# Kernel optimization log

Hardware: AMD Instinct MI355X
Metric: run time of the kernel (lower is better)

## Reference

```python
import jax, jax.numpy as jnp
import numpy as np

N_NEIGHBORS = 16


def setup_inputs() -> dict:
    key = jax.random.key(0)
    k1, k2 = jax.random.split(key)
    X_train = jax.random.normal(k1, (65536, 256), dtype=jnp.float32)
    X_test = jax.random.normal(k2, (4096, 256), dtype=jnp.float32)
    return {"X_train": X_train, "X_test": X_test}


def reference(X_train, X_test):
    # Euclidean cdist via ||a||^2 + ||b||^2 - 2 a.b (GEMM-dominant form)
    test_sq = jnp.sum(X_test * X_test, axis=1, keepdims=True)        # [Nt, 1]
    train_sq = jnp.sum(X_train * X_train, axis=1)[None, :]            # [1, Nn]
    cross = X_test @ X_train.T                                        # [Nt, Nn]
    d2 = jnp.maximum(test_sq + train_sq - 2.0 * cross, 0.0)
    dists = jnp.sqrt(d2)                                              # [Nt, Nn]
    # smallest-k == top_k of negated distances (returns ascending distances)
    _, idxs = jax.lax.top_k(-dists, N_NEIGHBORS)                      # [Nt, k]
    return idxs
```

## Files before the change

kernel.cpp:

```cpp
#include <hip/hip_runtime.h>
#include <hip/hip_bf16.h>


typedef short bf16x8 __attribute__((ext_vector_type(8)));
typedef float f32x4 __attribute__((ext_vector_type(4)));
typedef unsigned short ushort_t;
typedef unsigned long long u64;

#define K_DIM     256
#define N_TRAIN   65536
#define N_TEST    4096
#define TM        128
#define TN        128
#define NCHUNK    16
#define CHUNK_N   (N_TRAIN / NCHUNK)
#define ITERS     (CHUNK_N / TN)
#define LISTN     16
#define RPB       8
#define SENT      0xFFFFFFFFu

static __device__ __forceinline__ float np_pw_sq128(const float* __restrict__ x) {
    #pragma clang fp contract(off)
    float r0, r1, r2, r3, r4, r5, r6, r7;
    {
        const float4 a = *(const float4*)(x + 0);
        const float4 b = *(const float4*)(x + 4);
        r0 = a.x * a.x; r1 = a.y * a.y; r2 = a.z * a.z; r3 = a.w * a.w;
        r4 = b.x * b.x; r5 = b.y * b.y; r6 = b.z * b.z; r7 = b.w * b.w;
    }
    for (int i = 8; i < 128; i += 8) {
        const float4 a = *(const float4*)(x + i);
        const float4 b = *(const float4*)(x + i + 4);
        r0 = r0 + a.x * a.x; r1 = r1 + a.y * a.y;
        r2 = r2 + a.z * a.z; r3 = r3 + a.w * a.w;
        r4 = r4 + b.x * b.x; r5 = r5 + b.y * b.y;
        r6 = r6 + b.z * b.z; r7 = r7 + b.w * b.w;
    }
    return ((r0 + r1) + (r2 + r3)) + ((r4 + r5) + (r6 + r7));
}

static __device__ __forceinline__ void gld_lds16(const ushort_t* g, ushort_t* l) {
    __builtin_amdgcn_global_load_lds(
        (const __attribute__((address_space(1))) unsigned int*)g,
        (__attribute__((address_space(3))) unsigned int*)l,
        16, 0, 0);
}

static __device__ __forceinline__ ushort_t f2bf(float x) {
    unsigned u = __float_as_uint(x);
    return (ushort_t)((u + 0x7FFFu + ((u >> 16) & 1u)) >> 16);
}

__global__ __launch_bounds__(256) void convert_bf16(
    const float* __restrict__ src, ushort_t* __restrict__ dst, int nrows)
{
    const int wid = threadIdx.x >> 6, lane = threadIdx.x & 63;
    const int row = blockIdx.x * 4 + wid;
    if (row >= nrows) return;
    const float4 f = *(const float4*)(src + (size_t)row * K_DIM + lane * 4);
    ushort4 h;
    h.x = f2bf(f.x); h.y = f2bf(f.y); h.z = f2bf(f.z); h.w = f2bf(f.w);
    *(ushort4*)(dst + (size_t)row * K_DIM + lane * 4) = h;
}

__global__ __launch_bounds__(256) void train_sq_np(
    const float* __restrict__ train, float* __restrict__ bsq)
{
    const int r = blockIdx.x * 256 + threadIdx.x;
    const float* x = train + (size_t)r * K_DIM;
    bsq[r] = np_pw_sq128(x) + np_pw_sq128(x + 128);
}

__global__ __launch_bounds__(512, 4) void knn_approx(
    const ushort_t* __restrict__ testBf, const ushort_t* __restrict__ trainBf,
    const float* __restrict__ bsq, unsigned* __restrict__ cand)
{
    __shared__ __align__(16) ushort_t sB[TN * 128];
    __shared__ __align__(16) float    sBsq[TN];

    const int tid = threadIdx.x;
    const int bx = blockIdx.x;
    const int chunk = bx & (NCHUNK - 1);
    const int rowTile = bx >> 4;
    const int rowBase = rowTile * TM;
    const int chunkBase = chunk * CHUNK_N;
    const int lane = tid & 63;
    const int wid = tid >> 6;
    const int quad = lane >> 4;
    const int l15 = lane & 15;

    const int myRow = rowBase + wid * 16 + l15;

    unsigned lk[LISTN];
    #pragma unroll
    for (int j = 0; j < LISTN; ++j) lk[j] = 0x7F7FF000u | (unsigned)j;

    auto cins = [&](unsigned k) {
        if (k < lk[LISTN - 1]) {
            lk[LISTN - 1] = k;
            #pragma unroll
            for (int j = LISTN - 1; j > 0; --j)
                if (lk[j] < lk[j - 1]) {
                    const unsigned t = lk[j]; lk[j] = lk[j - 1]; lk[j - 1] = t;
                }
        }
    };

    unsigned q0 = SENT, q1 = SENT, q2 = SENT, q3 = SENT;
    float cutFp = __uint_as_float((lk[LISTN - 1] & 0xFFFFF000u) + 0x1000u);

    bf16x8 af[2][4];
    {
        const ushort_t* a0 = testBf + (size_t)myRow * K_DIM + quad * 8;
        #pragma unroll
        for (int p = 0; p < 2; ++p)
            #pragma unroll
            for (int s2 = 0; s2 < 4; ++s2)
                af[p][s2] = *(const bf16x8*)(a0 + p * 128 + s2 * 32);
    }

    const int rt = tid >> 4;
    const int ub = tid & 15;
    const int kg = ((ub & 7) ^ (rt & 7)) | (ub & 8);

    for (int it = 0; it < ITERS; ++it) {
        const int colBase = chunkBase + it * TN;
        f32x4 acc[8] = {};

        #pragma unroll
        for (int p = 0; p < 2; ++p) {
            __syncthreads();
            {
                const ushort_t* gb = trainBf + (size_t)(colBase + rt) * K_DIM + p * 128 + kg * 8;
                ushort_t* lb = sB + (size_t)tid * 8;
                #pragma unroll
                for (int c = 0; c < 4; ++c)
                    gld_lds16(gb + (size_t)c * 32 * K_DIM, lb + (size_t)c * 4096);
            }
            if (p == 0 && tid < TN) sBsq[tid] = bsq[colBase + tid] + 1024.0f;
            __syncthreads();

            #pragma unroll
            for (int s2 = 0; s2 < 4; ++s2) {
                #pragma unroll
                for (int ct = 0; ct < 8; ++ct) {
                    const int col = ct * 16 + l15;
                    const int g = s2 * 4 + quad;
                    const int pg = ((g & 7) ^ (col & 7)) | (g & 8);
                    const bf16x8 bfr = *(const bf16x8*)(sB + (size_t)col * 128 + pg * 8);
                    acc[ct] = __builtin_amdgcn_mfma_f32_16x16x32_bf16(bfr, af[p][s2], acc[ct], 0, 0, 0);
                }
            }
        }

        #pragma unroll
        for (int ct = 0; ct < 8; ++ct) {
            const float4 bq4 = *(const float4*)(sBsq + ct * 16 + quad * 4);
            const unsigned colb = (unsigned)(it * TN + ct * 16 + quad * 4);
            #pragma unroll
            for (int r = 0; r < 4; ++r) {
                const float bq = (r == 0) ? bq4.x : (r == 1) ? bq4.y : (r == 2) ? bq4.z : bq4.w;
                const float v = fmaf(-2.0f, acc[ct][r], bq);
                if (v < cutFp) {
                    cins(q3);
                    q3 = q2; q2 = q1; q1 = q0;
                    q0 = (__float_as_uint(v) & 0xFFFFF000u) | (colb + (unsigned)r);
                }
            }
        }

        cins(q3); cins(q2); cins(q1); cins(q0);
        q0 = SENT; q1 = SENT; q2 = SENT; q3 = SENT;
        cutFp = __uint_as_float((lk[LISTN - 1] & 0xFFFFF000u) + 0x1000u);
    }

    #pragma unroll
    for (int step = 16; step <= 32; step <<= 1) {
        unsigned other[LISTN];
        #pragma unroll
        for (int j = 0; j < LISTN; ++j)
            other[j] = (unsigned)__shfl_xor((int)lk[j], step, 64);
        unsigned c[LISTN];
        #pragma unroll
        for (int j = 0; j < LISTN; ++j) {
            const unsigned a = lk[j], b = other[LISTN - 1 - j];
            c[j] = a < b ? a : b;
        }
        #pragma unroll
        for (int d = 8; d >= 1; d >>= 1)
            #pragma unroll
            for (int j = 0; j < LISTN; ++j)
                if ((j & d) == 0) {
                    const unsigned x = c[j], y = c[j | d];
                    c[j] = x < y ? x : y;
                    c[j | d] = x < y ? y : x;
                }
        #pragma unroll
        for (int j = 0; j < LISTN; ++j) lk[j] = c[j];
    }

    if (lane < 16) {
        unsigned* dst = cand + (size_t)myRow * (NCHUNK * LISTN) + chunk * LISTN;
        #pragma unroll
        for (int j = 0; j < LISTN; ++j) dst[j] = lk[j];
    }
}

__global__ __launch_bounds__(256) void knn_refine(
    const float* __restrict__ test, const float* __restrict__ train,
    const float* __restrict__ bsq, const unsigned* __restrict__ cand,
    int* __restrict__ out)
{
    __shared__ __align__(16) float sArow[RPB * K_DIM];
    __shared__ int sSel[RPB * 32];

    const int tid = threadIdx.x;
    const int rowBase = blockIdx.x * RPB;
    const int r = tid >> 5;
    const int sub = tid & 31;

    {
        const float4* src = (const float4*)(test + (size_t)rowBase * K_DIM);
        float4* dst = (float4*)sArow;
        dst[tid] = src[tid];
        dst[256 + tid] = src[256 + tid];
    }

    u64 ek[8];
    {
        const unsigned* cp = cand + (size_t)(rowBase + r) * 256 + sub * 8;
        #pragma unroll
        for (int j = 0; j < 8; ++j) {
            const unsigned k = cp[j];
            const int chunkId = (sub * 8 + j) >> 4;
            const unsigned gidx = (unsigned)(chunkId * CHUNK_N) + (k & 0xFFFu);
            ek[j] = ((u64)(k & 0xFFFFF000u) << 8) | gidx;
        }
    }
    __syncthreads();

    for (int sel = 0; sel < 32; ++sel) {
        u64 bk = ek[0];
        #pragma unroll
        for (int j = 1; j < 8; ++j) bk = (ek[j] < bk) ? ek[j] : bk;
        #pragma unroll
        for (int off = 16; off > 0; off >>= 1) {
            const u64 ok = __shfl_xor(bk, off, 32);
            bk = (ok < bk) ? ok : bk;
        }
        if (sub == 0) sSel[r * 32 + sel] = (int)(bk & 0xFFFFULL);
        #pragma unroll
        for (int j = 0; j < 8; ++j)
            if (ek[j] == bk) ek[j] = ~0ULL;
    }
    __syncthreads();

    const int gidx = sSel[r * 32 + sub];
    const float* arow = sArow + r * K_DIM;
    const float ta = np_pw_sq128(arow) + np_pw_sq128(arow + 128);
    const float tb = bsq[gidx];

    const float4* bp = (const float4*)(train + (size_t)gidx * K_DIM);
    const float4* ap = (const float4*)arow;
    float c = 0.0f;
    #pragma unroll 8
    for (int k = 0; k < K_DIM / 4; ++k) {
        const float4 a = ap[k];
        const float4 b = bp[k];
        c = fmaf(a.x, b.x, c); c = fmaf(a.y, b.y, c);
        c = fmaf(a.z, b.z, c); c = fmaf(a.w, b.w, c);
    }
    float d32;
    {
        #pragma clang fp contract(off)
        const float t = ta + tb;
        float s = t - 2.0f * c;
        s = fmaxf(s, 0.0f);
        d32 = sqrtf(s);
    }

    u64 fk = ((u64)__float_as_uint(d32) << 32) | (unsigned)gidx;
    for (int sel = 0; sel < 16; ++sel) {
        u64 bk = fk;
        #pragma unroll
        for (int off = 16; off > 0; off >>= 1) {
            const u64 ok = __shfl_xor(bk, off, 32);
            bk = (ok < bk) ? ok : bk;
        }
        if (sub == 0) out[(size_t)(rowBase + r) * 16 + sel] = (int)(bk & 0xFFFFFFFFULL);
        if (fk == bk) fk = ~0ULL;
    }
}

extern "C" void kernel_launch(void* const* d_in, const int* in_sizes, int n_in,
                              void* d_out, int out_size, void* d_ws, size_t ws_size,
                              hipStream_t stream)
{
    const float* Xtrain = (const float*)d_in[0];
    const float* Xtest  = (const float*)d_in[1];
    int* out = (int*)d_out;

    const size_t OFF_TRAINBF = 0;
    const size_t OFF_TESTBF  = 33554432;
    const size_t OFF_BSQ     = 35651584;
    const size_t OFF_CAND    = 35913728;
    const size_t NEED        = 40108032;
    if (ws_size < NEED) return;

    char* ws = (char*)d_ws;
    ushort_t* trainBf = (ushort_t*)(ws + OFF_TRAINBF);
    ushort_t* testBf  = (ushort_t*)(ws + OFF_TESTBF);
    float*    bsq     = (float*)(ws + OFF_BSQ);
    unsigned* cand    = (unsigned*)(ws + OFF_CAND);

    convert_bf16<<<dim3(N_TRAIN / 4), dim3(256), 0, stream>>>(Xtrain, trainBf, N_TRAIN);
    convert_bf16<<<dim3(N_TEST / 4), dim3(256), 0, stream>>>(Xtest, testBf, N_TEST);
    train_sq_np<<<dim3(N_TRAIN / 256), dim3(256), 0, stream>>>(Xtrain, bsq);
    knn_approx<<<dim3((N_TEST / TM) * NCHUNK), dim3(512), 0, stream>>>(testBf, trainBf, bsq, cand);
    knn_refine<<<dim3(N_TEST / RPB), dim3(256), 0, stream>>>(Xtest, Xtrain, bsq, cand, out);
}
```

Measured before the change: 410.1 us.

## Switch KNN distance GEMM to 32x32x16 MFMA with 2D wave tiling

Replaces the 16x16x32 MFMA tiles with 32x32x16 bf16 MFMA. The 8 waves now form a 2x4 grid over a smaller 64-row tile, so each wave holds a 32x32 output block. The shared-memory layout for train tiles becomes k-group-major with unswizzled loads, and candidate queue flushes happen every other iteration. Per-wave partial top-16 lists are merged through shared memory with a 4-way merge before being written out. The aim is fewer LDS reads per MFMA and less insertion-sort overhead. The cost is halving the test rows per block, which doubles train-tile reloads, and possible LDS bank conflicts from the unswizzled layout.

```diff
diff --git a/kernel.cpp b/kernel.cpp
--- a/kernel.cpp
+++ b/kernel.cpp
@@ -3,14 +3,14 @@
 
 
 typedef short bf16x8 __attribute__((ext_vector_type(8)));
-typedef float f32x4 __attribute__((ext_vector_type(4)));
+typedef float f32x16 __attribute__((ext_vector_type(16)));
 typedef unsigned short ushort_t;
 typedef unsigned long long u64;
 
 #define K_DIM     256
 #define N_TRAIN   65536
 #define N_TEST    4096
-#define TM        128
+#define TM        64
 #define TN        128
 #define NCHUNK    16
 #define CHUNK_N   (N_TRAIN / NCHUNK)
@@ -75,7 +75,7 @@
     const ushort_t* __restrict__ testBf, const ushort_t* __restrict__ trainBf,
     const float* __restrict__ bsq, unsigned* __restrict__ cand)
 {
-    __shared__ __align__(16) ushort_t sB[TN * 128];
+    __shared__ __align__(16) ushort_t sB[16 * TN * 8];
     __shared__ __align__(16) float    sBsq[TN];
 
     const int tid = threadIdx.x;
@@ -86,10 +86,12 @@
     const int chunkBase = chunk * CHUNK_N;
     const int lane = tid & 63;
     const int wid = tid >> 6;
-    const int quad = lane >> 4;
-    const int l15 = lane & 15;
-
-    const int myRow = rowBase + wid * 16 + l15;
+    const int rg = wid >> 2;
+    const int cg = wid & 3;
+    const int l31 = lane & 31;
+    const int hi = lane >> 5;
+
+    const int myRow = rowBase + rg * 32 + l31;
 
     unsigned lk[LISTN];
     #pragma unroll
@@ -109,77 +111,73 @@
     unsigned q0 = SENT, q1 = SENT, q2 = SENT, q3 = SENT;
     float cutFp = __uint_as_float((lk[LISTN - 1] & 0xFFFFF000u) + 0x1000u);
 
-    bf16x8 af[2][4];
-    {
-        const ushort_t* a0 = testBf + (size_t)myRow * K_DIM + quad * 8;
-        #pragma unroll
-        for (int p = 0; p < 2; ++p)
-            #pragma unroll
-            for (int s2 = 0; s2 < 4; ++s2)
-                af[p][s2] = *(const bf16x8*)(a0 + p * 128 + s2 * 32);
-    }
-
-    const int rt = tid >> 4;
-    const int ub = tid & 15;
-    const int kg = ((ub & 7) ^ (rt & 7)) | (ub & 8);
+    bf16x8 af[16];
+    {
+        const ushort_t* a0 = testBf + (size_t)myRow * K_DIM + hi * 8;
+        #pragma unroll
+        for (int s = 0; s < 16; ++s)
+            af[s] = *(const bf16x8*)(a0 + s * 16);
+    }
+
+    const int scol = tid & 127;
+    const int sgb  = tid >> 7;
 
     for (int it = 0; it < ITERS; ++it) {
         const int colBase = chunkBase + it * TN;
-        f32x4 acc[8] = {};
+        f32x16 acc = {};
 
         #pragma unroll
         for (int p = 0; p < 2; ++p) {
             __syncthreads();
             {
-                const ushort_t* gb = trainBf + (size_t)(colBase + rt) * K_DIM + p * 128 + kg * 8;
+                const ushort_t* gb = trainBf + (size_t)(colBase + scol) * K_DIM + p * 128 + sgb * 8;
                 ushort_t* lb = sB + (size_t)tid * 8;
                 #pragma unroll
                 for (int c = 0; c < 4; ++c)
-                    gld_lds16(gb + (size_t)c * 32 * K_DIM, lb + (size_t)c * 4096);
+                    gld_lds16(gb + (size_t)c * 32, lb + (size_t)c * 4096);
             }
             if (p == 0 && tid < TN) sBsq[tid] = bsq[colBase + tid] + 1024.0f;
             __syncthreads();
 
             #pragma unroll
-            for (int s2 = 0; s2 < 4; ++s2) {
-                #pragma unroll
-                for (int ct = 0; ct < 8; ++ct) {
-                    const int col = ct * 16 + l15;
-                    const int g = s2 * 4 + quad;
-                    const int pg = ((g & 7) ^ (col & 7)) | (g & 8);
-                    const bf16x8 bfr = *(const bf16x8*)(sB + (size_t)col * 128 + pg * 8);
-                    acc[ct] = __builtin_amdgcn_mfma_f32_16x16x32_bf16(bfr, af[p][s2], acc[ct], 0, 0, 0);
-                }
+            for (int sp = 0; sp < 8; ++sp) {
+                const int g = sp * 2 + hi;
+                const bf16x8 ta = *(const bf16x8*)(sB + ((size_t)g * TN + cg * 32 + l31) * 8);
+                acc = __builtin_amdgcn_mfma_f32_32x32x16_bf16(ta, af[p * 8 + sp], acc, 0, 0, 0);
             }
         }
 
-        #pragma unroll
-        for (int ct = 0; ct < 8; ++ct) {
-            const float4 bq4 = *(const float4*)(sBsq + ct * 16 + quad * 4);
-            const unsigned colb = (unsigned)(it * TN + ct * 16 + quad * 4);
-            #pragma unroll
-            for (int r = 0; r < 4; ++r) {
-                const float bq = (r == 0) ? bq4.x : (r == 1) ? bq4.y : (r == 2) ? bq4.z : bq4.w;
-                const float v = fmaf(-2.0f, acc[ct][r], bq);
-                if (v < cutFp) {
-                    cins(q3);
-                    q3 = q2; q2 = q1; q1 = q0;
-                    q0 = (__float_as_uint(v) & 0xFFFFF000u) | (colb + (unsigned)r);
-                }
+        const float* bqb = sBsq + cg * 32 + hi * 4;
+        const float4 bq0 = *(const float4*)(bqb + 0);
+        const float4 bq1 = *(const float4*)(bqb + 8);
+        const float4 bq2 = *(const float4*)(bqb + 16);
+        const float4 bq3 = *(const float4*)(bqb + 24);
+        const unsigned colb = (unsigned)(it * TN + cg * 32 + hi * 4);
+        #pragma unroll
+        for (int r = 0; r < 16; ++r) {
+            const float4 bq4 = (r < 4) ? bq0 : (r < 8) ? bq1 : (r < 12) ? bq2 : bq3;
+            const int rr = r & 3;
+            const float bq = (rr == 0) ? bq4.x : (rr == 1) ? bq4.y : (rr == 2) ? bq4.z : bq4.w;
+            const float v = fmaf(-2.0f, acc[r], bq);
+            if (v < cutFp) {
+                cins(q3);
+                q3 = q2; q2 = q1; q1 = q0;
+                q0 = (__float_as_uint(v) & 0xFFFFF000u) | (colb + (unsigned)(r & 3) + 8u * (unsigned)(r >> 2));
             }
         }
 
-        cins(q3); cins(q2); cins(q1); cins(q0);
-        q0 = SENT; q1 = SENT; q2 = SENT; q3 = SENT;
-        cutFp = __uint_as_float((lk[LISTN - 1] & 0xFFFFF000u) + 0x1000u);
-    }
-
-    #pragma unroll
-    for (int step = 16; step <= 32; step <<= 1) {
+        if (it & 1) {
+            cins(q3); cins(q2); cins(q1); cins(q0);
+            q0 = SENT; q1 = SENT; q2 = SENT; q3 = SENT;
+            cutFp = __uint_as_float((lk[LISTN - 1] & 0xFFFFF000u) + 0x1000u);
+        }
+    }
+
+    {
         unsigned other[LISTN];
         #pragma unroll
         for (int j = 0; j < LISTN; ++j)
-            other[j] = (unsigned)__shfl_xor((int)lk[j], step, 64);
+            other[j] = (unsigned)__shfl_xor((int)lk[j], 32, 64);
         unsigned c[LISTN];
         #pragma unroll
         for (int j = 0; j < LISTN; ++j) {
@@ -199,10 +197,35 @@
         for (int j = 0; j < LISTN; ++j) lk[j] = c[j];
     }
 
-    if (lane < 16) {
-        unsigned* dst = cand + (size_t)myRow * (NCHUNK * LISTN) + chunk * LISTN;
+    __syncthreads();
+    unsigned* scr = (unsigned*)sB;
+    if (lane < 32) {
+        unsigned* dst = scr + ((size_t)wid * 32 + l31) * LISTN;
         #pragma unroll
         for (int j = 0; j < LISTN; ++j) dst[j] = lk[j];
+    }
+    __syncthreads();
+    if (tid < TM) {
+        const int rgo = tid >> 5;
+        const int r32 = tid & 31;
+        const unsigned* L0 = scr + ((size_t)(rgo * 4 + 0) * 32 + r32) * LISTN;
+        const unsigned* L1 = scr + ((size_t)(rgo * 4 + 1) * 32 + r32) * LISTN;
+        const unsigned* L2 = scr + ((size_t)(rgo * 4 + 2) * 32 + r32) * LISTN;
+        const unsigned* L3 = scr + ((size_t)(rgo * 4 + 3) * 32 + r32) * LISTN;
+        unsigned* dst = cand + (size_t)(rowBase + tid) * (NCHUNK * LISTN) + chunk * LISTN;
+        int i0 = 0, i1 = 0, i2 = 0, i3 = 0;
+        #pragma unroll
+        for (int j = 0; j < LISTN; ++j) {
+            const unsigned v0 = L0[i0], v1 = L1[i1], v2 = L2[i2], v3 = L3[i3];
+            const unsigned m01 = v0 < v1 ? v0 : v1;
+            const unsigned m23 = v2 < v3 ? v2 : v3;
+            const unsigned m = m01 < m23 ? m01 : m23;
+            dst[j] = m;
+            if (v0 == m)      ++i0;
+            else if (v1 == m) ++i1;
+            else if (v2 == m) ++i2;
+            else              ++i3;
+        }
     }
 }
 
```

New measurement: 591.3 us. 44.2% more time.
